# Optimization experiments

Hardware: AMD Instinct MI355X
Metric: run time of the kernel (lower is better)

Reference implementation:

```python
import jax, jax.numpy as jnp
import numpy as np

# qshift_a: Kingsbury 10-tap Q-shift filters (sum(h0a) = sqrt(2)).
_H0A = np.array([0.0351638365171441, 0.0, -0.0883294244510729,
                 0.233890320607236, 0.760272369066126, 0.587518297723561,
                 0.0, -0.114301837144249, 0.0, 0.0], dtype=np.float64)
_H0B = _H0A[::-1].copy()
_ALT = (-1.0) ** np.arange(10)
_H1A = _H0B * _ALT            # highpass tree a
_H1B = _H1A[::-1].copy()
# synthesis filters (g0a = h0b, g0b = h0a, g1a = h1b, g1b = h1a)
G0A = _H0B.astype(np.float32)
G0B = _H0A.astype(np.float32)
G1A = _H1B.astype(np.float32)
G1B = _H1A.astype(np.float32)


def _reflect(x, minx, maxx):
    # dtcwt symmetric-extension index reflection (static, numpy)
    x = np.asarray(x, dtype=np.float64)
    rng = maxx - minx
    rng2 = 2.0 * rng
    mod = np.fmod(x - minx, rng2)
    normed = np.where(mod < 0, mod + rng2, mod)
    out = np.where(normed >= rng, rng2 - normed, normed) + minx
    return out.astype(np.int64)


def _colifilt(X, ha, hb):
    # X: (B, C, r, c) -> (B, C, 2r, c). ha, hb are 1-D numpy filters (static).
    m = ha.shape[0]
    m2 = m // 2
    assert m2 % 2 == 1, 'implemented for 10/14/18-tap qshift (m/2 odd)'
    b, ch, r, c = X.shape
    r2 = r // 2
    xe = _reflect(np.arange(-m2, r + m2), -0.5, r - 0.5)   # static indices
    t = np.arange(2, r + m - 1, 2)
    if float(np.sum(ha * hb)) > 0:
        ta, tb = t, t - 1
    else:
        ta, tb = t - 1, t
    Xa = X[:, :, xe[ta], :]   # (B, C, r/2 + m/2 - 1, c)
    Xb = X[:, :, xe[tb], :]
    hao, hae = ha[0::2], ha[1::2]
    hbo, hbe = hb[0::2], hb[1::2]

    def vconv(Z, h):
        # valid convolution along dim 2 (true conv: filter flipped)
        hf = h[::-1]
        out = Z[:, :, 0:r2, :] * float(hf[0])
        for k in range(1, m2):
            out = out + Z[:, :, k:k + r2, :] * float(hf[k])
        return out

    y = jnp.stack([vconv(Xb, hao), vconv(Xa, hbo),
                   vconv(Xb, hae), vconv(Xa, hbe)], axis=3)  # (B,C,r/2,4,c)
    return y.reshape(b, ch, 2 * r, c)


def _rowifilt(X, ha, hb):
    return jnp.swapaxes(_colifilt(jnp.swapaxes(X, 2, 3), ha, hb), 2, 3)


def _c2q(wr, wi):
    # complex pair of subbands -> real quad image. wr, wi: (B, C, 2, H, W) -> (B, C, 2H, 2W)
    w1r, w2r = wr[:, :, 0], wr[:, :, 1]
    w1i, w2i = wi[:, :, 0], wi[:, :, 1]
    x1 = w1r + w2r
    x2 = w1i + w2i
    x3 = w1i - w2i
    x4 = w2r - w1r
    b, c, h, w = x1.shape
    top = jnp.stack([x1, x2], axis=-1).reshape(b, c, h, 2 * w)
    bot = jnp.stack([x3, x4], axis=-1).reshape(b, c, h, 2 * w)
    y = jnp.stack([top, bot], axis=-2).reshape(b, c, 2 * h, 2 * w)
    return y * np.float32(1.0 / np.sqrt(2.0))


def setup_inputs() -> dict:
    key = jax.random.key(0)
    k1, k2, k3 = jax.random.split(key, 3)
    B, C, H, W = 8, 64, 128, 128
    Yl = jax.random.normal(k1, (B, C, H, W), dtype=jnp.float32)
    Yhr = jax.random.normal(k2, (B, C, 6, H // 2, W // 2), dtype=jnp.float32)
    Yhi = jax.random.normal(k3, (B, C, 6, H // 2, W // 2), dtype=jnp.float32)
    return {"Yl": Yl, "Yhr": Yhr, "Yhi": Yhi}


def reference(Yl, Yhr, Yhi):
    lh = _c2q(Yhr[:, :, 0:6:5], Yhi[:, :, 0:6:5])
    hl = _c2q(Yhr[:, :, 2:4:1], Yhi[:, :, 2:4:1])
    hh = _c2q(Yhr[:, :, 1:5:3], Yhi[:, :, 1:5:3])
    y1 = _rowifilt(Yl, G0B, G0A) + _rowifilt(hl, G1B, G1A)
    y2 = _rowifilt(lh, G0B, G0A) + _rowifilt(hh, G1B, G1A)
    return _colifilt(y1, G0B, G0A) + _colifilt(y2, G1B, G1A)
```

## Files before the change

### kernel.cpp

```cpp
#include <hip/hip_runtime.h>

#define NTHREADS 256

typedef float v2f __attribute__((ext_vector_type(2)));

__device__ __forceinline__ int reflect128(int p) {
    p = (p < 0) ? (-p - 1) : p;
    p = (p >= 128) ? (255 - p) : p;
    return p;
}

__constant__ int   cs0[4] = {2, 1, 1, 0};
__constant__ int   cs1[4] = {1, 2, 0, 1};
__constant__ float cc0[4][3] = {
    { 0.760272369066126f, -0.0883294244510729f,  0.0351638365171441f},
    { 0.233890320607236f,  0.587518297723561f,  -0.114301837144249f},
    {-0.114301837144249f,  0.587518297723561f,   0.233890320607236f},
    { 0.0351638365171441f, -0.0883294244510729f, 0.760272369066126f}};
__constant__ float cc1[4][3] = {
    { 0.233890320607236f,  0.587518297723561f,  -0.114301837144249f},
    {-0.760272369066126f,  0.0883294244510729f, -0.0351638365171441f},
    {-0.0351638365171441f, 0.0883294244510729f, -0.760272369066126f},
    {-0.114301837144249f,  0.587518297723561f,   0.233890320607236f}};

static constexpr int   kcs0[4] = {2, 1, 1, 0};
static constexpr int   kcs1[4] = {1, 2, 0, 1};
static constexpr float kcc0[4][3] = {
    { 0.760272369066126f, -0.0883294244510729f,  0.0351638365171441f},
    { 0.233890320607236f,  0.587518297723561f,  -0.114301837144249f},
    {-0.114301837144249f,  0.587518297723561f,   0.233890320607236f},
    { 0.0351638365171441f, -0.0883294244510729f, 0.760272369066126f}};
static constexpr float kcc1[4][3] = {
    { 0.233890320607236f,  0.587518297723561f,  -0.114301837144249f},
    {-0.760272369066126f,  0.0883294244510729f, -0.0351638365171441f},
    {-0.0351638365171441f, 0.0883294244510729f, -0.760272369066126f},
    {-0.114301837144249f,  0.587518297723561f,   0.233890320607236f}};

__global__ __launch_bounds__(NTHREADS, 6)
void dtcwt_inv_kernel(const float* __restrict__ Yl,
                      const float* __restrict__ Yhr,
                      const float* __restrict__ Yhi,
                      float* __restrict__ out)
{
    const int tid = threadIdx.x;

    const int bid  = blockIdx.x;
    const int perx = gridDim.x >> 3;
    const int gidx = (bid & 7) * perx + (bid >> 3);
    const int plane = gidx >> 4;
    const int tile  = gidx & 15;
    const int ct = tile & 3;
    const int rt = tile >> 2;

    const int OR0 = rt * 64, OC0 = ct * 64;
    const int i0r = OR0 >> 2, i0c = OC0 >> 2;
    const int yrb = 2 * i0r - 4;
    const int icb = 2 * i0c - 4;

    const float* yl = Yl + (size_t)plane * (128 * 128);
    const float* hr = Yhr + (size_t)plane * 6 * 4096;
    const float* hi = Yhi + (size_t)plane * 6 * 4096;

    __shared__ v2f sP[40][40];
    __shared__ v2f sQ[40][40];

    const float RS2 = 0.70710678118654752440f;

#pragma unroll
    for (int k = 0; k < 4; ++k) {
        const int e = tid + k * NTHREADS;
        if (k == 3 && e >= 800) break;
        const int t  = e / 20;
        const int u2 = e - t * 20;
        const int ry = reflect128(yrb + t);
        const int cr0 = icb + 2 * u2;
        int base; int swap;
        if (cr0 < 0)        { base = -cr0 - 2;  swap = 1; }
        else if (cr0 > 126) { base = 254 - cr0; swap = 1; }
        else                { base = cr0;       swap = 0; }
        const float2 v = *(const float2*)(yl + ry * 128 + base);
        sP[t][2 * u2].x     = swap ? v.y : v.x;
        sP[t][2 * u2 + 1].x = swap ? v.x : v.y;
    }

    {
        const int e0 = tid;
        const int e1 = tid + NTHREADS;
        const int has1 = (e1 < 400);

        const int t2a = e0 / 20, u2a = e0 - t2a * 20;
        const int ara = i0r - 2 + t2a, aca = i0c - 2 + u2a;
        const int oobra = (ara < 0) | (ara >= 64);
        const int oobca = (aca < 0) | (aca >= 64);
        const int r2a = oobra ? ((ara < 0) ? (-ara - 1) : (127 - ara)) : ara;
        const int c2a = oobca ? ((aca < 0) ? (-aca - 1) : (127 - aca)) : aca;
        const int offa = r2a * 64 + c2a;

        const int e1c = has1 ? e1 : 0;
        const int t2b = e1c / 20, u2b = e1c - t2b * 20;
        const int arb = i0r - 2 + t2b, acb = i0c - 2 + u2b;
        const int oobrb = (arb < 0) | (arb >= 64);
        const int oobcb = (acb < 0) | (acb >= 64);
        const int r2b = oobrb ? ((arb < 0) ? (-arb - 1) : (127 - arb)) : arb;
        const int c2b = oobcb ? ((acb < 0) ? (-acb - 1) : (127 - acb)) : acb;
        const int offb = r2b * 64 + c2b;

        float Ra[6], Ia[6], Rb[6], Ib[6];
#pragma unroll
        for (int k = 0; k < 6; ++k) { Ra[k] = hr[k * 4096 + offa]; Ia[k] = hi[k * 4096 + offa]; }
#pragma unroll
        for (int k = 0; k < 6; ++k) { Rb[k] = hr[k * 4096 + offb]; Ib[k] = hi[k * 4096 + offb]; }

#pragma unroll
        for (int wq = 0; wq < 2; ++wq) {
            if (wq == 1 && !has1) break;
            const float* R = (wq == 0) ? Ra : Rb;
            const float* I = (wq == 0) ? Ia : Ib;
            const int t2 = (wq == 0) ? t2a : t2b;
            const int u2 = (wq == 0) ? u2a : u2b;
            const int oobr = (wq == 0) ? oobra : oobrb;
            const int oobc = (wq == 0) ? oobca : oobcb;
#pragma unroll
            for (int dt = 0; dt < 2; ++dt) {
#pragma unroll
                for (int du = 0; du < 2; ++du) {
                    const int p = dt ^ oobr;
                    const int q = du ^ oobc;
                    const float sA = (p & q) ? -RS2 : RS2;
                    const float sB = (p & (q ^ 1)) ? -RS2 : RS2;
                    float b0, b5, b2v, b3, b1, b4;
                    if (p == q) { b0 = R[0]; b5 = R[5]; b2v = R[2]; b3 = R[3]; b1 = R[1]; b4 = R[4]; }
                    else        { b0 = I[0]; b5 = I[5]; b2v = I[2]; b3 = I[3]; b1 = I[1]; b4 = I[4]; }
                    const int t = 2 * t2 + dt, u = 2 * u2 + du;
                    sP[t][u].y = sA * b0 + sB * b5;
                    v2f qv; qv.x = sA * b2v + sB * b3;
                    qv.y = sA * b1 + sB * b4;
                    sQ[t][u] = qv;
                }
            }
        }
    }
    __syncthreads();

    const int c  = tid & 63;
    const int g  = tid >> 6;
    const int jc = c & 3;
    const int q2 = c >> 2;
    const float a0  = cc0[jc][0], a1  = cc0[jc][1], a2  = cc0[jc][2];
    const float b0w = cc1[jc][0], b1w = cc1[jc][1], b2w = cc1[jc][2];
    const int ub0 = 2 * q2 + (jc & 1) + 2 * cs0[jc];
    const int ub1 = 2 * q2 + ((jc & 1) ^ 1) + 2 * cs1[jc];

    const int tb = 8 * g;
    float y1v[14], y2v[14];
#pragma unroll
    for (int k = 0; k < 14; ++k) {
        const int t = tb + 1 + k;
        const v2f acc = sP[t][ub0] * a0  + sP[t][ub0 + 2] * a1  + sP[t][ub0 + 4] * a2
                      + sQ[t][ub1] * b0w + sQ[t][ub1 + 2] * b1w + sQ[t][ub1 + 4] * b2w;
        y1v[k] = acc.x;
        y2v[k] = acc.y;
    }

    float* op = out + ((size_t)plane * 256 + OR0 + 16 * g) * 256 + OC0 + c;
#pragma unroll
    for (int j = 0; j < 4; ++j) {
        constexpr int P0c[4] = {0, 1, 0, 1};
        const int p0 = P0c[j], p1 = p0 ^ 1;
        const int r0 = p0 + 2 * kcs0[j];
        const int r1 = p1 + 2 * kcs1[j];
        const float d0 = kcc0[j][0], d1 = kcc0[j][1], d2 = kcc0[j][2];
        const float e0 = kcc1[j][0], e1 = kcc1[j][1], e2 = kcc1[j][2];
#pragma unroll
        for (int mm = 0; mm < 4; ++mm) {
            const int k0 = 2 * mm + r0 - 1;
            const int k1 = 2 * mm + r1 - 1;
            const float acc = y1v[k0] * d0 + y1v[k0 + 2] * d1 + y1v[k0 + 4] * d2
                            + y2v[k1] * e0 + y2v[k1 + 2] * e1 + y2v[k1 + 4] * e2;
            op[(size_t)(4 * mm + j) * 256] = acc;
        }
    }
}

extern "C" void kernel_launch(void* const* d_in, const int* in_sizes, int n_in,
                              void* d_out, int out_size, void* d_ws, size_t ws_size,
                              hipStream_t stream) {
    const float* Yl  = (const float*)d_in[0];
    const float* Yhr = (const float*)d_in[1];
    const float* Yhi = (const float*)d_in[2];
    float* out = (float*)d_out;

    const int planes = in_sizes[0] / (128 * 128);
    dim3 grid(planes * 16, 1, 1);
    dtcwt_inv_kernel<<<grid, NTHREADS, 0, stream>>>(Yl, Yhr, Yhi, out);
}
```

Before: 254.2 us.

## Give each wavefront a private shared-memory slice and drop the block barrier

Each wavefront now loads and transforms only the 14 intermediate rows it needs into its own shared-memory slice. The block-wide __syncthreads is replaced by an lgkmcnt wait plus a wave barrier. Yl is read as float4 instead of float2, and the launch-bounds occupancy hint drops from 6 to 4. Overlapping halo rows between wavefronts are now loaded and computed redundantly, trading extra global reads and ALU work for no inter-wave synchronisation.

```diff
diff --git a/kernel.cpp b/kernel.cpp
--- a/kernel.cpp
+++ b/kernel.cpp
@@ -36,13 +36,15 @@
     {-0.0351638365171441f, 0.0883294244510729f, -0.760272369066126f},
     {-0.114301837144249f,  0.587518297723561f,   0.233890320607236f}};
 
-__global__ __launch_bounds__(NTHREADS, 6)
+__global__ __launch_bounds__(NTHREADS, 4)
 void dtcwt_inv_kernel(const float* __restrict__ Yl,
                       const float* __restrict__ Yhr,
                       const float* __restrict__ Yhi,
                       float* __restrict__ out)
 {
-    const int tid = threadIdx.x;
+    const int tid  = threadIdx.x;
+    const int lane = tid & 63;
+    const int g    = tid >> 6;
 
     const int bid  = blockIdx.x;
     const int perx = gridDim.x >> 3;
@@ -61,44 +63,55 @@
     const float* hr = Yhr + (size_t)plane * 6 * 4096;
     const float* hi = Yhi + (size_t)plane * 6 * 4096;
 
-    __shared__ v2f sP[40][40];
-    __shared__ v2f sQ[40][40];
+    __shared__ v2f sP[4][14][40];
+    __shared__ v2f sQ[4][14][40];
+    v2f (*wP)[40] = sP[g];
+    v2f (*wQ)[40] = sQ[g];
 
     const float RS2 = 0.70710678118654752440f;
 
-#pragma unroll
-    for (int k = 0; k < 4; ++k) {
-        const int e = tid + k * NTHREADS;
-        if (k == 3 && e >= 800) break;
-        const int t  = e / 20;
-        const int u2 = e - t * 20;
+    float4 f4[3];
+    int trow[3], u4[3];
+#pragma unroll
+    for (int s = 0; s < 3; ++s) {
+        const int idx = lane + s * 64;
+        const int ok = (s < 2) | (idx < 140);
+        const int idc = ok ? idx : 0;
+        trow[s] = idc / 10;
+        u4[s]   = idc - trow[s] * 10;
+        const int t  = 8 * g + 1 + trow[s];
         const int ry = reflect128(yrb + t);
-        const int cr0 = icb + 2 * u2;
-        int base; int swap;
-        if (cr0 < 0)        { base = -cr0 - 2;  swap = 1; }
-        else if (cr0 > 126) { base = 254 - cr0; swap = 1; }
-        else                { base = cr0;       swap = 0; }
-        const float2 v = *(const float2*)(yl + ry * 128 + base);
-        sP[t][2 * u2].x     = swap ? v.y : v.x;
-        sP[t][2 * u2 + 1].x = swap ? v.x : v.y;
+        const int cr0 = icb + 4 * u4[s];
+        int base, rev;
+        if (cr0 < 0)        { base = -cr0 - 4;  rev = 1; }
+        else if (cr0 > 124) { base = 252 - cr0; rev = 1; }
+        else                { base = cr0;       rev = 0; }
+        const float4 v = *(const float4*)(yl + ry * 128 + base);
+        f4[s].x = rev ? v.w : v.x;
+        f4[s].y = rev ? v.z : v.y;
+        f4[s].z = rev ? v.y : v.z;
+        f4[s].w = rev ? v.x : v.w;
+        if (ok) {
+            wP[trow[s]][4 * u4[s] + 0].x = f4[s].x;
+            wP[trow[s]][4 * u4[s] + 1].x = f4[s].y;
+            wP[trow[s]][4 * u4[s] + 2].x = f4[s].z;
+            wP[trow[s]][4 * u4[s] + 3].x = f4[s].w;
+        }
     }
 
     {
-        const int e0 = tid;
-        const int e1 = tid + NTHREADS;
-        const int has1 = (e1 < 400);
-
-        const int t2a = e0 / 20, u2a = e0 - t2a * 20;
-        const int ara = i0r - 2 + t2a, aca = i0c - 2 + u2a;
+        const int q0 = lane, q1 = lane + 64;
+        const int t2a = q0 / 20, u2a = q0 - t2a * 20;
+        const int t2b = q1 / 20, u2b = q1 - t2b * 20;
+
+        const int ara = i0r - 2 + 4 * g + t2a, aca = i0c - 2 + u2a;
         const int oobra = (ara < 0) | (ara >= 64);
         const int oobca = (aca < 0) | (aca >= 64);
         const int r2a = oobra ? ((ara < 0) ? (-ara - 1) : (127 - ara)) : ara;
         const int c2a = oobca ? ((aca < 0) ? (-aca - 1) : (127 - aca)) : aca;
         const int offa = r2a * 64 + c2a;
 
-        const int e1c = has1 ? e1 : 0;
-        const int t2b = e1c / 20, u2b = e1c - t2b * 20;
-        const int arb = i0r - 2 + t2b, acb = i0c - 2 + u2b;
+        const int arb = i0r - 2 + 4 * g + t2b, acb = i0c - 2 + u2b;
         const int oobrb = (arb < 0) | (arb >= 64);
         const int oobcb = (acb < 0) | (acb >= 64);
         const int r2b = oobrb ? ((arb < 0) ? (-arb - 1) : (127 - arb)) : arb;
@@ -113,37 +126,73 @@
 
 #pragma unroll
         for (int wq = 0; wq < 2; ++wq) {
-            if (wq == 1 && !has1) break;
             const float* R = (wq == 0) ? Ra : Rb;
             const float* I = (wq == 0) ? Ia : Ib;
-            const int t2 = (wq == 0) ? t2a : t2b;
-            const int u2 = (wq == 0) ? u2a : u2b;
+            const int t2l = (wq == 0) ? t2a : t2b;
+            const int u2  = (wq == 0) ? u2a : u2b;
             const int oobr = (wq == 0) ? oobra : oobrb;
             const int oobc = (wq == 0) ? oobca : oobcb;
 #pragma unroll
             for (int dt = 0; dt < 2; ++dt) {
+                const int tl = 2 * t2l + dt - 1;
+                if (tl < 0 || tl >= 14) continue;
+                const int p = dt ^ oobr;
 #pragma unroll
                 for (int du = 0; du < 2; ++du) {
-                    const int p = dt ^ oobr;
                     const int q = du ^ oobc;
                     const float sA = (p & q) ? -RS2 : RS2;
                     const float sB = (p & (q ^ 1)) ? -RS2 : RS2;
                     float b0, b5, b2v, b3, b1, b4;
                     if (p == q) { b0 = R[0]; b5 = R[5]; b2v = R[2]; b3 = R[3]; b1 = R[1]; b4 = R[4]; }
                     else        { b0 = I[0]; b5 = I[5]; b2v = I[2]; b3 = I[3]; b1 = I[1]; b4 = I[4]; }
-                    const int t = 2 * t2 + dt, u = 2 * u2 + du;
-                    sP[t][u].y = sA * b0 + sB * b5;
+                    const int u = 2 * u2 + du;
+                    wP[tl][u].y = sA * b0 + sB * b5;
                     v2f qv; qv.x = sA * b2v + sB * b3;
                     qv.y = sA * b1 + sB * b4;
-                    sQ[t][u] = qv;
+                    wQ[tl][u] = qv;
                 }
             }
         }
-    }
-    __syncthreads();
-
-    const int c  = tid & 63;
-    const int g  = tid >> 6;
+
+        if (lane < 32) {
+            const int q2i = lane + 128;
+            const int t2c = q2i / 20, u2c = q2i - t2c * 20;
+            const int arc = i0r - 2 + 4 * g + t2c, acc_ = i0c - 2 + u2c;
+            const int oobrc = (arc < 0) | (arc >= 64);
+            const int oobcc = (acc_ < 0) | (acc_ >= 64);
+            const int r2c = oobrc ? ((arc < 0) ? (-arc - 1) : (127 - arc)) : arc;
+            const int c2c = oobcc ? ((acc_ < 0) ? (-acc_ - 1) : (127 - acc_)) : acc_;
+            const int offc = r2c * 64 + c2c;
+            float Rc[6], Ic[6];
+#pragma unroll
+            for (int k = 0; k < 6; ++k) { Rc[k] = hr[k * 4096 + offc]; Ic[k] = hi[k * 4096 + offc]; }
+#pragma unroll
+            for (int dt = 0; dt < 2; ++dt) {
+                const int tl = 2 * t2c + dt - 1;
+                if (tl < 0 || tl >= 14) continue;
+                const int p = dt ^ oobrc;
+#pragma unroll
+                for (int du = 0; du < 2; ++du) {
+                    const int q = du ^ oobcc;
+                    const float sA = (p & q) ? -RS2 : RS2;
+                    const float sB = (p & (q ^ 1)) ? -RS2 : RS2;
+                    float b0, b5, b2v, b3, b1, b4;
+                    if (p == q) { b0 = Rc[0]; b5 = Rc[5]; b2v = Rc[2]; b3 = Rc[3]; b1 = Rc[1]; b4 = Rc[4]; }
+                    else        { b0 = Ic[0]; b5 = Ic[5]; b2v = Ic[2]; b3 = Ic[3]; b1 = Ic[1]; b4 = Ic[4]; }
+                    const int u = 2 * u2c + du;
+                    wP[tl][u].y = sA * b0 + sB * b5;
+                    v2f qv; qv.x = sA * b2v + sB * b3;
+                    qv.y = sA * b1 + sB * b4;
+                    wQ[tl][u] = qv;
+                }
+            }
+        }
+    }
+
+    asm volatile("s_waitcnt lgkmcnt(0)" ::: "memory");
+    __builtin_amdgcn_wave_barrier();
+
+    const int c  = lane;
     const int jc = c & 3;
     const int q2 = c >> 2;
     const float a0  = cc0[jc][0], a1  = cc0[jc][1], a2  = cc0[jc][2];
@@ -151,13 +200,11 @@
     const int ub0 = 2 * q2 + (jc & 1) + 2 * cs0[jc];
     const int ub1 = 2 * q2 + ((jc & 1) ^ 1) + 2 * cs1[jc];
 
-    const int tb = 8 * g;
     float y1v[14], y2v[14];
 #pragma unroll
     for (int k = 0; k < 14; ++k) {
-        const int t = tb + 1 + k;
-        const v2f acc = sP[t][ub0] * a0  + sP[t][ub0 + 2] * a1  + sP[t][ub0 + 4] * a2
-                      + sQ[t][ub1] * b0w + sQ[t][ub1 + 2] * b1w + sQ[t][ub1 + 4] * b2w;
+        const v2f acc = wP[k][ub0] * a0  + wP[k][ub0 + 2] * a1  + wP[k][ub0 + 4] * a2
+                      + wQ[k][ub1] * b0w + wQ[k][ub1 + 2] * b1w + wQ[k][ub1 + 4] * b2w;
         y1v[k] = acc.x;
         y2v[k] = acc.y;
     }
```

New measurement: 255.9 us. About the same (+0.7%).
